# Kernel tuning notes

Hardware: AMD Instinct MI355X
Metric: run time of the kernel (lower is better)

Reference implementation:

```python
import jax, jax.numpy as jnp
import numpy as np

N_WL = 296      # spectral points after dropping last 4
POOL = 4
FM = N_WL // POOL  # 74
HEAD = 64
EMB = 48


def setup_inputs() -> dict:
    key = jax.random.key(0)
    ks = jax.random.split(key, 16)
    B = 2048
    inp = {
        "x": jax.random.uniform(ks[0], (B, 300), dtype=jnp.float32),
        # FeaturePicker DI
        "wDI": jax.random.normal(ks[1], (HEAD, FM, FM), dtype=jnp.float32),
        "bDI": jax.random.normal(ks[2], (HEAD,), dtype=jnp.float32),
        "fcDI_w": jax.random.normal(ks[3], (EMB, HEAD), dtype=jnp.float32) * 0.1,
        "fcDI_b": jax.random.normal(ks[4], (EMB,), dtype=jnp.float32) * 0.1,
        # FeaturePicker NDI
        "wNDI": jax.random.normal(ks[5], (HEAD, FM, FM), dtype=jnp.float32),
        "bNDI": jax.random.normal(ks[6], (HEAD,), dtype=jnp.float32),
        "fcNDI_w": jax.random.normal(ks[7], (EMB, HEAD), dtype=jnp.float32) * 0.1,
        "fcNDI_b": jax.random.normal(ks[8], (EMB,), dtype=jnp.float32) * 0.1,
        # head MLP
        "fc1_w": jax.random.normal(ks[9], (48, 96), dtype=jnp.float32) * 0.1,
        "fc1_b": jax.random.normal(ks[10], (48,), dtype=jnp.float32) * 0.1,
        "l1_w": jax.random.normal(ks[11], (20, 48), dtype=jnp.float32) * 0.1,
        "l1_b": jax.random.normal(ks[12], (20,), dtype=jnp.float32) * 0.1,
        "l2_w": jax.random.normal(ks[13], (1, 20), dtype=jnp.float32) * 0.1,
        "l2_b": jax.random.normal(ks[14], (1,), dtype=jnp.float32) * 0.1,
    }
    return inp


def _feature_picker(m, wmap, bias, fw, fb):
    # m: [B, 296, 296] -> avgpool 4x4 -> [B, 74, 74]
    B = m.shape[0]
    p = m.reshape(B, FM, POOL, FM, POOL).mean(axis=(2, 4))
    # weighted sum against each of HEAD weight maps (== [B,5476] @ [5476,HEAD])
    h = jnp.einsum('bij,hij->bh', p, wmap) + bias
    h = jax.nn.elu(h)
    return jax.nn.elu(h @ fw.T + fb)  # [B, EMB]


def reference(x, wDI, bDI, fcDI_w, fcDI_b, wNDI, bNDI, fcNDI_w, fcNDI_b,
              fc1_w, fc1_b, l1_w, l1_b, l2_w, l2_b):
    x0 = x[:, :-4]                       # [B, 296]
    a = x0[:, None, :]                   # unsqueeze(1)
    b = x0[:, :, None]                   # unsqueeze(2)
    DI = a - b                           # [B, 296, 296]
    NDI = (a - b) / (a + b + 1e-5)
    eDI = _feature_picker(DI, wDI, bDI, fcDI_w, fcDI_b)
    eNDI = _feature_picker(NDI, wNDI, bNDI, fcNDI_w, fcNDI_b)
    emb = jnp.concatenate([eDI, eNDI], axis=1)      # [B, 96]
    emb = jax.nn.elu(emb @ fc1_w.T + fc1_b)
    emb = jax.nn.elu(emb @ l1_w.T + l1_b)
    return jax.nn.sigmoid(emb @ l2_w.T + l2_b)      # [B, 1]
```

## Files before the change

kernel.cpp:

```cpp
#include <hip/hip_runtime.h>
#include <hip/hip_bf16.h>
#include <math.h>

#define NWL    296
#define FMD    74
#define HEAD   64
#define EMBD   48
#define BATCH  2048
#define XCOLS  300
#define NPAIR  2701
#define NPAIR_P 3072
#define KSPLIT 4
#define SEGLEN (NPAIR_P / KSPLIT)
#define KCH    256
#define MROWS  16
#define TB     8

#define WS_CMR  0
#define WS_PAIR (FMD * HEAD)
#define WS_PDI  (WS_PAIR + NPAIR_P)
#define WS_PNDI (WS_PDI + BATCH * HEAD)
#define WS_WATT (WS_PNDI + KSPLIT * BATCH * HEAD)

typedef _Float16 f16x8 __attribute__((ext_vector_type(8)));
typedef float f32x4 __attribute__((ext_vector_type(4)));

__device__ __forceinline__ float eluf(float x) { return x > 0.f ? x : expm1f(x); }

__device__ __forceinline__ void pair_decode(int k, int& I, int& J) {
  I = (int)((147.0f - sqrtf(21609.0f - 8.0f * (float)k)) * 0.5f);
  int base = (I * (147 - I)) >> 1;
  while (base > k) { I--; base = (I * (147 - I)) >> 1; }
  while (I < 72 && ((I + 1) * (146 - I)) / 2 <= k) { I++; base = (I * (147 - I)) >> 1; }
  J = I + 1 + (k - base);
}

__global__ __launch_bounds__(256) void fcr_prep_v4(
    const float* __restrict__ wDI,
    const float* __restrict__ wNDI,
    float* __restrict__ ws) {
  __shared__ float wdL[FMD * FMD];
  __shared__ float wnL[FMD * FMD];

  int t = threadIdx.x;
  int h = blockIdx.x;

  const float4* gd = (const float4*)(wDI + (size_t)h * FMD * FMD);
  const float4* gn = (const float4*)(wNDI + (size_t)h * FMD * FMD);
  for (int i = t; i < FMD * FMD / 4; i += 256) {
    ((float4*)wdL)[i] = gd[i];
    ((float4*)wnL)[i] = gn[i];
  }
  __syncthreads();

  _Float16* wATt = (_Float16*)(ws + WS_WATT);
  for (int k = t; k < NPAIR_P; k += 256) {
    float v = 0.f;
    if (k < NPAIR) {
      int I, J; pair_decode(k, I, J);
      v = (wnL[I * FMD + J] - wnL[J * FMD + I]) * 0.0625f;
    }
    wATt[(size_t)h * NPAIR_P + k] = (_Float16)v;
  }

  if (t < FMD) {
    int K = t;
    float cs = 0.f, rs = 0.f;
    for (int I = 0; I < FMD; I++) {
      cs += wdL[I * FMD + K];
      rs += wdL[K * FMD + I];
    }
    ws[WS_CMR + K * 64 + h] = cs - rs;
  }

  if (h == 0) {
    unsigned* P = (unsigned*)(ws + WS_PAIR);
    for (int k = t; k < NPAIR_P; k += 256) {
      unsigned pb = 0;
      if (k < NPAIR) {
        int I, J; pair_decode(k, I, J);
        pb = (unsigned)(4 * I) | ((unsigned)(4 * J) << 16);
      }
      P[k] = pb;
    }
  }
}

__global__ __launch_bounds__(256) void fcr_main_v4(
    const float* __restrict__ x,
    float* __restrict__ ws) {
  __shared__ float xs[MROWS][308];
  __shared__ float xs4[MROWS][FMD];
  __shared__ _Float16 Sm[MROWS][264];
  __shared__ unsigned pairsL[SEGLEN];

  const unsigned* pairG = (const unsigned*)(ws + WS_PAIR);
  const _Float16* wATt = (const _Float16*)(ws + WS_WATT);
  const float* cmr = ws + WS_CMR;
  float* pDI  = ws + WS_PDI;
  float* pNDI = ws + WS_PNDI;

  int t = threadIdx.x;
  int seg = blockIdx.x & (KSPLIT - 1);
  int row0 = (blockIdx.x >> 2) * MROWS;
  int k0 = seg * SEGLEN;

  for (int i = t; i < MROWS * (NWL / 4); i += 256) {
    int r = i / (NWL / 4), c4 = i - r * (NWL / 4);
    *(float4*)&xs[r][4 * c4] = *(const float4*)(x + (size_t)(row0 + r) * XCOLS + 4 * c4);
  }
  for (int i = t; i < SEGLEN; i += 256) pairsL[i] = pairG[k0 + i];
  __syncthreads();

  for (int i = t; i < MROWS * FMD; i += 256) {
    int r = i / FMD, K = i - r * FMD;
    xs4[r][K] = 0.25f * (xs[r][4*K] + xs[r][4*K+1] + xs[r][4*K+2] + xs[r][4*K+3]);
  }
  __syncthreads();

  int lane = t & 63;
  int wv   = t >> 6;
  int n_in = lane & 15;
  int quad = lane >> 4;
  int h    = wv * 16 + n_in;

  if (seg == 0) {
    int g = wv;
    float a0 = 0.f, a1 = 0.f, a2 = 0.f, a3 = 0.f;
    int hh = lane;
    for (int K = 0; K < FMD; K++) {
      float w = cmr[K * 64 + hh];
      a0 = fmaf(xs4[g*4+0][K], w, a0);
      a1 = fmaf(xs4[g*4+1][K], w, a1);
      a2 = fmaf(xs4[g*4+2][K], w, a2);
      a3 = fmaf(xs4[g*4+3][K], w, a3);
    }
    pDI[(size_t)(row0 + g*4 + 0) * 64 + hh] = a0;
    pDI[(size_t)(row0 + g*4 + 1) * 64 + hh] = a1;
    pDI[(size_t)(row0 + g*4 + 2) * 64 + hh] = a2;
    pDI[(size_t)(row0 + g*4 + 3) * 64 + hh] = a3;
  }

  f32x4 acc = {0.f, 0.f, 0.f, 0.f};
  int mA = t & 15;
  int kg = t >> 4;

  for (int chunk = 0; chunk < SEGLEN / KCH; chunk++) {
    #pragma unroll 4
    for (int j = 0; j < 16; j++) {
      int kc = kg * 16 + j;
      unsigned pb = pairsL[chunk * KCH + kc];
      int bI = pb & 0xFFFF, bJ = pb >> 16;
      float4 uv = *(const float4*)&xs[mA][bJ];
      float4 vv = *(const float4*)&xs[mA][bI];
      float u2[4] = { fmaf(2.f, uv.x, 1e-5f), fmaf(2.f, uv.y, 1e-5f),
                      fmaf(2.f, uv.z, 1e-5f), fmaf(2.f, uv.w, 1e-5f) };
      float u[4]  = { uv.x, uv.y, uv.z, uv.w };
      float v[4]  = { vv.x, vv.y, vv.z, vv.w };
      float s = 0.f;
      #pragma unroll
      for (int a = 0; a < 4; a++) {
        float va = v[a] + 1e-5f;
        #pragma unroll
        for (int b = 0; b < 4; b++)
          s = fmaf(u2[b], __builtin_amdgcn_rcpf(u[b] + va), s);
      }
      Sm[mA][kc] = (_Float16)(s - 16.f);
    }
    __syncthreads();

    int kbase = k0 + chunk * KCH;
    #pragma unroll
    for (int c = 0; c < KCH / 32; c++) {
      f16x8 aF = *(const f16x8*)&Sm[n_in][c * 32 + quad * 8];
      f16x8 bF = *(const f16x8*)&wATt[(size_t)h * NPAIR_P + kbase + c * 32 + quad * 8];
      acc = __builtin_amdgcn_mfma_f32_16x16x32_f16(aF, bF, acc, 0, 0, 0);
    }
    __syncthreads();
  }

  #pragma unroll
  for (int r = 0; r < 4; r++) {
    int m = quad * 4 + r;
    pNDI[((size_t)seg * BATCH + row0 + m) * 64 + h] = acc[r];
  }
}

__global__ __launch_bounds__(256) void fcr_tail_v4(
    const float* __restrict__ ws,
    const float* __restrict__ bDI,
    const float* __restrict__ fcDI_w,
    const float* __restrict__ fcDI_b,
    const float* __restrict__ bNDI,
    const float* __restrict__ fcNDI_w,
    const float* __restrict__ fcNDI_b,
    const float* __restrict__ fc1_w,
    const float* __restrict__ fc1_b,
    const float* __restrict__ l1_w,
    const float* __restrict__ l1_b,
    const float* __restrict__ l2_w,
    const float* __restrict__ l2_b,
    float* __restrict__ out) {
  __shared__ float wDT[HEAD * EMBD];
  __shared__ float wNT[HEAD * EMBD];
  __shared__ float w1T[96 * 48];
  __shared__ float wl1T[48 * 20];
  __shared__ float wl2s[20];
  __shared__ float bD[HEAD], bN[HEAD], bDe[EMBD], bNe[EMBD], b1[48], bl1s[20];
  __shared__ float bl2s;
  __shared__ float ehD[TB][68], ehN[TB][68];
  __shared__ float e2[TB][100];
  __shared__ float e3[TB][52];
  __shared__ float e4[TB][20];

  int t = threadIdx.x;
  for (int i = t; i < HEAD * EMBD; i += 256) {
    int o = i >> 6, hh = i & 63;
    wDT[hh * EMBD + o] = fcDI_w[i];
    wNT[hh * EMBD + o] = fcNDI_w[i];
  }
  for (int i = t; i < 48 * 96; i += 256) {
    int o = i / 96, j = i - o * 96;
    w1T[j * 48 + o] = fc1_w[i];
  }
  for (int i = t; i < 20 * 48; i += 256) {
    int o = i / 48, j = i - o * 48;
    wl1T[j * 20 + o] = l1_w[i];
  }
  if (t < 20)   { wl2s[t] = l2_w[t]; bl1s[t] = l1_b[t]; }
  if (t < HEAD) { bD[t] = bDI[t]; bN[t] = bNDI[t]; }
  if (t < EMBD) { bDe[t] = fcDI_b[t]; bNe[t] = fcNDI_b[t]; }
  if (t < 48)   b1[t] = fc1_b[t];
  if (t == 0)   bl2s = l2_b[0];

  const float* pDI  = ws + WS_PDI;
  const float* pNDI = ws + WS_PNDI;
  int row0 = blockIdx.x * TB;
  __syncthreads();

  for (int i = t; i < TB * HEAD; i += 256) {
    int r = i >> 6, hh = i & 63;
    int row = row0 + r;
    float hD = pDI[(size_t)row * 64 + hh] + bD[hh];
    float hN = bN[hh];
    for (int s2 = 0; s2 < KSPLIT; s2++)
      hN += pNDI[((size_t)s2 * BATCH + row) * 64 + hh];
    ehD[r][hh] = eluf(hD);
    ehN[r][hh] = eluf(hN);
  }
  __syncthreads();

  for (int i = t; i < TB * 96; i += 256) {
    int r = i / 96, o = i - r * 96;
    int isN = o >= 48;
    int o2 = isN ? o - 48 : o;
    const float* wb = isN ? wNT : wDT;
    const float* eb = isN ? &ehN[r][0] : &ehD[r][0];
    float s = isN ? bNe[o2] : bDe[o2];
    for (int hh = 0; hh < 64; hh++)
      s = fmaf(eb[hh], wb[hh * EMBD + o2], s);
    e2[r][o] = eluf(s);
  }
  __syncthreads();

  for (int i = t; i < TB * 48; i += 256) {
    int r = i / 48, o = i - r * 48;
    float s = b1[o];
    for (int j = 0; j < 96; j++)
      s = fmaf(e2[r][j], w1T[j * 48 + o], s);
    e3[r][o] = eluf(s);
  }
  __syncthreads();

  if (t < TB * 20) {
    int r = t / 20, o = t - r * 20;
    float s = bl1s[o];
    for (int j = 0; j < 48; j++)
      s = fmaf(e3[r][j], wl1T[j * 20 + o], s);
    e4[r][o] = eluf(s);
  }
  __syncthreads();

  if (t < TB) {
    float s = bl2s;
    for (int j = 0; j < 20; j++)
      s = fmaf(e4[t][j], wl2s[j], s);
    out[row0 + t] = 1.f / (1.f + expf(-s));
  }
}

extern "C" void kernel_launch(void* const* d_in, const int* in_sizes, int n_in,
                              void* d_out, int out_size, void* d_ws, size_t ws_size,
                              hipStream_t stream) {
  const float* x      = (const float*)d_in[0];
  const float* wDI    = (const float*)d_in[1];
  const float* bDI    = (const float*)d_in[2];
  const float* fcDI_w = (const float*)d_in[3];
  const float* fcDI_b = (const float*)d_in[4];
  const float* wNDI   = (const float*)d_in[5];
  const float* bNDI   = (const float*)d_in[6];
  const float* fcNDI_w= (const float*)d_in[7];
  const float* fcNDI_b= (const float*)d_in[8];
  const float* fc1_w  = (const float*)d_in[9];
  const float* fc1_b  = (const float*)d_in[10];
  const float* l1_w   = (const float*)d_in[11];
  const float* l1_b   = (const float*)d_in[12];
  const float* l2_w   = (const float*)d_in[13];
  const float* l2_b   = (const float*)d_in[14];
  float* out = (float*)d_out;
  float* ws = (float*)d_ws;

  fcr_prep_v4<<<HEAD, 256, 0, stream>>>(wDI, wNDI, ws);
  fcr_main_v4<<<(BATCH / MROWS) * KSPLIT, 256, 0, stream>>>(x, ws);
  fcr_tail_v4<<<BATCH / TB, 256, 0, stream>>>(ws, bDI, fcDI_w, fcDI_b,
      bNDI, fcNDI_w, fcNDI_b, fc1_w, fc1_b, l1_w, l1_b, l2_w, l2_b, out);
}
```

Baseline: 133.2 us.

## Fuse main and tail kernels, drop K-split, process 8 rows per block

Merges the NDI MFMA kernel and the MLP tail into one kernel with 8 batch rows per block and no K-split. The pair table is read straight from global memory instead of being staged in LDS. This removes the partial-sum workspace round trip and one launch, and tail weights are stored in LDS as fp16. In exchange, half of each 16-row MFMA tile is wasted on duplicated rows, and every block now loads the tail weights and the full wATt stream for its rows. Grid size drops to 256 blocks, which lowers parallelism.

```diff
diff --git a/kernel.cpp b/kernel.cpp
--- a/kernel.cpp
+++ b/kernel.cpp
@@ -10,17 +10,12 @@
 #define XCOLS  300
 #define NPAIR  2701
 #define NPAIR_P 3072
-#define KSPLIT 4
-#define SEGLEN (NPAIR_P / KSPLIT)
-#define KCH    256
-#define MROWS  16
-#define TB     8
+#define KCH    768
+#define MR     8
 
 #define WS_CMR  0
 #define WS_PAIR (FMD * HEAD)
-#define WS_PDI  (WS_PAIR + NPAIR_P)
-#define WS_PNDI (WS_PDI + BATCH * HEAD)
-#define WS_WATT (WS_PNDI + KSPLIT * BATCH * HEAD)
+#define WS_WATT (WS_PAIR + NPAIR_P)
 
 typedef _Float16 f16x8 __attribute__((ext_vector_type(8)));
 typedef float f32x4 __attribute__((ext_vector_type(4)));
@@ -35,7 +30,7 @@
   J = I + 1 + (k - base);
 }
 
-__global__ __launch_bounds__(256) void fcr_prep_v4(
+__global__ __launch_bounds__(256) void fcr_prep_v5(
     const float* __restrict__ wDI,
     const float* __restrict__ wNDI,
     float* __restrict__ ws) {
@@ -86,70 +81,102 @@
   }
 }
 
-__global__ __launch_bounds__(256) void fcr_main_v4(
+__global__ __launch_bounds__(256) void fcr_fused_v5(
     const float* __restrict__ x,
-    float* __restrict__ ws) {
-  __shared__ float xs[MROWS][308];
-  __shared__ float xs4[MROWS][FMD];
-  __shared__ _Float16 Sm[MROWS][264];
-  __shared__ unsigned pairsL[SEGLEN];
+    const float* __restrict__ ws,
+    const float* __restrict__ bDI,
+    const float* __restrict__ fcDI_w,
+    const float* __restrict__ fcDI_b,
+    const float* __restrict__ bNDI,
+    const float* __restrict__ fcNDI_w,
+    const float* __restrict__ fcNDI_b,
+    const float* __restrict__ fc1_w,
+    const float* __restrict__ fc1_b,
+    const float* __restrict__ l1_w,
+    const float* __restrict__ l1_b,
+    const float* __restrict__ l2_w,
+    const float* __restrict__ l2_b,
+    float* __restrict__ out) {
+  __shared__ float xs[MR][308];
+  __shared__ float xs4[MR][FMD];
+  __shared__ _Float16 Sm[MR][776];
+  __shared__ _Float16 wDT[HEAD * EMBD];
+  __shared__ _Float16 wNT[HEAD * EMBD];
+  __shared__ _Float16 w1T[96 * 48];
+  __shared__ _Float16 wl1T[48 * 20];
+  __shared__ float wl2s[20];
+  __shared__ float bDs[HEAD], bNs[HEAD], bDe[EMBD], bNe[EMBD], b1[48], bl1s[20];
+  __shared__ float bl2s;
+  __shared__ float ehD[MR][68], ehN[MR][68];
+  __shared__ float e2[MR][100];
+  __shared__ float e3[MR][52];
+  __shared__ float e4[MR][20];
 
   const unsigned* pairG = (const unsigned*)(ws + WS_PAIR);
   const _Float16* wATt = (const _Float16*)(ws + WS_WATT);
   const float* cmr = ws + WS_CMR;
-  float* pDI  = ws + WS_PDI;
-  float* pNDI = ws + WS_PNDI;
 
   int t = threadIdx.x;
-  int seg = blockIdx.x & (KSPLIT - 1);
-  int row0 = (blockIdx.x >> 2) * MROWS;
-  int k0 = seg * SEGLEN;
-
-  for (int i = t; i < MROWS * (NWL / 4); i += 256) {
+  int row0 = blockIdx.x * MR;
+
+  for (int i = t; i < MR * (NWL / 4); i += 256) {
     int r = i / (NWL / 4), c4 = i - r * (NWL / 4);
     *(float4*)&xs[r][4 * c4] = *(const float4*)(x + (size_t)(row0 + r) * XCOLS + 4 * c4);
   }
-  for (int i = t; i < SEGLEN; i += 256) pairsL[i] = pairG[k0 + i];
-  __syncthreads();
-
-  for (int i = t; i < MROWS * FMD; i += 256) {
+  for (int i = t; i < HEAD * EMBD; i += 256) {
+    int o = i >> 6, hh = i & 63;
+    wDT[hh * EMBD + o] = (_Float16)fcDI_w[i];
+    wNT[hh * EMBD + o] = (_Float16)fcNDI_w[i];
+  }
+  for (int i = t; i < 48 * 96; i += 256) {
+    int o = i / 96, j = i - o * 96;
+    w1T[j * 48 + o] = (_Float16)fc1_w[i];
+  }
+  for (int i = t; i < 20 * 48; i += 256) {
+    int o = i / 48, j = i - o * 48;
+    wl1T[j * 20 + o] = (_Float16)l1_w[i];
+  }
+  if (t < 20)   { wl2s[t] = l2_w[t]; bl1s[t] = l1_b[t]; }
+  if (t < HEAD) { bDs[t] = bDI[t]; bNs[t] = bNDI[t]; }
+  if (t < EMBD) { bDe[t] = fcDI_b[t]; bNe[t] = fcNDI_b[t]; }
+  if (t < 48)   b1[t] = fc1_b[t];
+  if (t == 0)   bl2s = l2_b[0];
+  __syncthreads();
+
+  for (int i = t; i < MR * FMD; i += 256) {
     int r = i / FMD, K = i - r * FMD;
     xs4[r][K] = 0.25f * (xs[r][4*K] + xs[r][4*K+1] + xs[r][4*K+2] + xs[r][4*K+3]);
   }
   __syncthreads();
+
+  {
+    int hh = t & 63, g = t >> 6;
+    float d0 = 0.f, d1 = 0.f;
+    for (int K = 0; K < FMD; K++) {
+      float w = cmr[K * 64 + hh];
+      d0 = fmaf(xs4[2*g][K],   w, d0);
+      d1 = fmaf(xs4[2*g+1][K], w, d1);
+    }
+    ehD[2*g][hh]   = eluf(d0 + bDs[hh]);
+    ehD[2*g+1][hh] = eluf(d1 + bDs[hh]);
+  }
 
   int lane = t & 63;
   int wv   = t >> 6;
   int n_in = lane & 15;
   int quad = lane >> 4;
   int h    = wv * 16 + n_in;
-
-  if (seg == 0) {
-    int g = wv;
-    float a0 = 0.f, a1 = 0.f, a2 = 0.f, a3 = 0.f;
-    int hh = lane;
-    for (int K = 0; K < FMD; K++) {
-      float w = cmr[K * 64 + hh];
-      a0 = fmaf(xs4[g*4+0][K], w, a0);
-      a1 = fmaf(xs4[g*4+1][K], w, a1);
-      a2 = fmaf(xs4[g*4+2][K], w, a2);
-      a3 = fmaf(xs4[g*4+3][K], w, a3);
-    }
-    pDI[(size_t)(row0 + g*4 + 0) * 64 + hh] = a0;
-    pDI[(size_t)(row0 + g*4 + 1) * 64 + hh] = a1;
-    pDI[(size_t)(row0 + g*4 + 2) * 64 + hh] = a2;
-    pDI[(size_t)(row0 + g*4 + 3) * 64 + hh] = a3;
-  }
+  int mA   = t & 7;
+  int kg   = t >> 3;
 
   f32x4 acc = {0.f, 0.f, 0.f, 0.f};
-  int mA = t & 15;
-  int kg = t >> 4;
-
-  for (int chunk = 0; chunk < SEGLEN / KCH; chunk++) {
+
+  for (int chunk = 0; chunk < NPAIR_P / KCH; chunk++) {
+    int kbase = chunk * KCH;
     #pragma unroll 4
-    for (int j = 0; j < 16; j++) {
-      int kc = kg * 16 + j;
-      unsigned pb = pairsL[chunk * KCH + kc];
+    for (int j = 0; j < KCH / 32; j++) {
+      int kc = kg + 32 * j;
+      unsigned pb = pairG[kbase + kc];
       int bI = pb & 0xFFFF, bJ = pb >> 16;
       float4 uv = *(const float4*)&xs[mA][bJ];
       float4 vv = *(const float4*)&xs[mA][bI];
@@ -169,119 +196,56 @@
     }
     __syncthreads();
 
-    int kbase = k0 + chunk * KCH;
     #pragma unroll
     for (int c = 0; c < KCH / 32; c++) {
-      f16x8 aF = *(const f16x8*)&Sm[n_in][c * 32 + quad * 8];
+      f16x8 aF = *(const f16x8*)&Sm[n_in & 7][c * 32 + quad * 8];
       f16x8 bF = *(const f16x8*)&wATt[(size_t)h * NPAIR_P + kbase + c * 32 + quad * 8];
       acc = __builtin_amdgcn_mfma_f32_16x16x32_f16(aF, bF, acc, 0, 0, 0);
     }
     __syncthreads();
   }
 
-  #pragma unroll
-  for (int r = 0; r < 4; r++) {
-    int m = quad * 4 + r;
-    pNDI[((size_t)seg * BATCH + row0 + m) * 64 + h] = acc[r];
-  }
-}
-
-__global__ __launch_bounds__(256) void fcr_tail_v4(
-    const float* __restrict__ ws,
-    const float* __restrict__ bDI,
-    const float* __restrict__ fcDI_w,
-    const float* __restrict__ fcDI_b,
-    const float* __restrict__ bNDI,
-    const float* __restrict__ fcNDI_w,
-    const float* __restrict__ fcNDI_b,
-    const float* __restrict__ fc1_w,
-    const float* __restrict__ fc1_b,
-    const float* __restrict__ l1_w,
-    const float* __restrict__ l1_b,
-    const float* __restrict__ l2_w,
-    const float* __restrict__ l2_b,
-    float* __restrict__ out) {
-  __shared__ float wDT[HEAD * EMBD];
-  __shared__ float wNT[HEAD * EMBD];
-  __shared__ float w1T[96 * 48];
-  __shared__ float wl1T[48 * 20];
-  __shared__ float wl2s[20];
-  __shared__ float bD[HEAD], bN[HEAD], bDe[EMBD], bNe[EMBD], b1[48], bl1s[20];
-  __shared__ float bl2s;
-  __shared__ float ehD[TB][68], ehN[TB][68];
-  __shared__ float e2[TB][100];
-  __shared__ float e3[TB][52];
-  __shared__ float e4[TB][20];
-
-  int t = threadIdx.x;
-  for (int i = t; i < HEAD * EMBD; i += 256) {
-    int o = i >> 6, hh = i & 63;
-    wDT[hh * EMBD + o] = fcDI_w[i];
-    wNT[hh * EMBD + o] = fcNDI_w[i];
-  }
-  for (int i = t; i < 48 * 96; i += 256) {
-    int o = i / 96, j = i - o * 96;
-    w1T[j * 48 + o] = fc1_w[i];
-  }
-  for (int i = t; i < 20 * 48; i += 256) {
-    int o = i / 48, j = i - o * 48;
-    wl1T[j * 20 + o] = l1_w[i];
-  }
-  if (t < 20)   { wl2s[t] = l2_w[t]; bl1s[t] = l1_b[t]; }
-  if (t < HEAD) { bD[t] = bDI[t]; bN[t] = bNDI[t]; }
-  if (t < EMBD) { bDe[t] = fcDI_b[t]; bNe[t] = fcNDI_b[t]; }
-  if (t < 48)   b1[t] = fc1_b[t];
-  if (t == 0)   bl2s = l2_b[0];
-
-  const float* pDI  = ws + WS_PDI;
-  const float* pNDI = ws + WS_PNDI;
-  int row0 = blockIdx.x * TB;
-  __syncthreads();
-
-  for (int i = t; i < TB * HEAD; i += 256) {
-    int r = i >> 6, hh = i & 63;
-    int row = row0 + r;
-    float hD = pDI[(size_t)row * 64 + hh] + bD[hh];
-    float hN = bN[hh];
-    for (int s2 = 0; s2 < KSPLIT; s2++)
-      hN += pNDI[((size_t)s2 * BATCH + row) * 64 + hh];
-    ehD[r][hh] = eluf(hD);
-    ehN[r][hh] = eluf(hN);
-  }
-  __syncthreads();
-
-  for (int i = t; i < TB * 96; i += 256) {
+  if (quad < 2) {
+    #pragma unroll
+    for (int r = 0; r < 4; r++) {
+      int m = quad * 4 + r;
+      ehN[m][h] = eluf(acc[r] + bNs[h]);
+    }
+  }
+  __syncthreads();
+
+  for (int i = t; i < MR * 96; i += 256) {
     int r = i / 96, o = i - r * 96;
     int isN = o >= 48;
     int o2 = isN ? o - 48 : o;
-    const float* wb = isN ? wNT : wDT;
+    const _Float16* wb = isN ? wNT : wDT;
     const float* eb = isN ? &ehN[r][0] : &ehD[r][0];
     float s = isN ? bNe[o2] : bDe[o2];
     for (int hh = 0; hh < 64; hh++)
-      s = fmaf(eb[hh], wb[hh * EMBD + o2], s);
+      s = fmaf(eb[hh], (float)wb[hh * EMBD + o2], s);
     e2[r][o] = eluf(s);
   }
   __syncthreads();
 
-  for (int i = t; i < TB * 48; i += 256) {
+  for (int i = t; i < MR * 48; i += 256) {
     int r = i / 48, o = i - r * 48;
     float s = b1[o];
     for (int j = 0; j < 96; j++)
-      s = fmaf(e2[r][j], w1T[j * 48 + o], s);
+      s = fmaf(e2[r][j], (float)w1T[j * 48 + o], s);
     e3[r][o] = eluf(s);
   }
   __syncthreads();
 
-  if (t < TB * 20) {
+  if (t < MR * 20) {
     int r = t / 20, o = t - r * 20;
     float s = bl1s[o];
     for (int j = 0; j < 48; j++)
-      s = fmaf(e3[r][j], wl1T[j * 20 + o], s);
+      s = fmaf(e3[r][j], (float)wl1T[j * 20 + o], s);
     e4[r][o] = eluf(s);
   }
   __syncthreads();
 
-  if (t < TB) {
+  if (t < MR) {
     float s = bl2s;
     for (int j = 0; j < 20; j++)
       s = fmaf(e4[t][j], wl2s[j], s);
@@ -310,8 +274,7 @@
   float* out = (float*)d_out;
   float* ws = (float*)d_ws;
 
-  fcr_prep_v4<<<HEAD, 256, 0, stream>>>(wDI, wNDI, ws);
-  fcr_main_v4<<<(BATCH / MROWS) * KSPLIT, 256, 0, stream>>>(x, ws);
-  fcr_tail_v4<<<BATCH / TB, 256, 0, stream>>>(ws, bDI, fcDI_w, fcDI_b,
+  fcr_prep_v5<<<HEAD, 256, 0, stream>>>(wDI, wNDI, ws);
+  fcr_fused_v5<<<BATCH / MR, 256, 0, stream>>>(x, ws, bDI, fcDI_w, fcDI_b,
       bNDI, fcNDI_w, fcNDI_b, fc1_w, fc1_b, l1_w, l1_b, l2_w, l2_b, out);
 }
```

Result: slower. 137.1 us (+2.9%).
